# Kernel tuning notes

Hardware: AMD Instinct MI355X
Metric: run time of the kernel (lower is better)

Reference implementation:

```python
import jax, jax.numpy as jnp
import numpy as np

N_BINS = 8  # grid resolution per axis -> R = 64 regions


def setup_inputs() -> dict:
    key = jax.random.key(0)
    ks = jax.random.split(key, 11)
    N, D, A, H = 100000, 1024, 128, 256
    s = 0.02
    return {
        "x": jax.random.normal(ks[0], (N, D), dtype=jnp.float32),
        "coords": jax.random.uniform(ks[1], (N, 2), dtype=jnp.float32),
        "U_w": jax.random.normal(ks[2], (A, D), dtype=jnp.float32) * s,
        "U_b": jnp.zeros((A,), jnp.float32),
        "V_w": jax.random.normal(ks[3], (A, D), dtype=jnp.float32) * s,
        "V_b": jnp.zeros((A,), jnp.float32),
        "w_w": jax.random.normal(ks[4], (1, A), dtype=jnp.float32) * s,
        "c1_w": jax.random.normal(ks[5], (H, D), dtype=jnp.float32) * s,
        "c1_b": jnp.zeros((H,), jnp.float32),
        "c2_w": jax.random.normal(ks[6], (1, H), dtype=jnp.float32) * s,
        "c2_b": jnp.zeros((1,), jnp.float32),
    }


def reference(x, coords, U_w, U_b, V_w, V_b, w_w, c1_w, c1_b, c2_w, c2_b):
    n = N_BINS
    R = n * n
    # --- spatial binning: [N,2] coords -> [N] region ids in [0, n^2) ---
    lo = coords.min(axis=0)
    hi = coords.max(axis=0)
    span = jnp.maximum(hi - lo, 1.0)
    bins = jnp.clip(((coords - lo) / span * n).astype(jnp.int32), 0, n - 1)
    rid = bins[:, 1] * n + bins[:, 0]  # [N]
    # --- segment mean (single O(N) sweep instead of per-region loops) ---
    sums = jax.ops.segment_sum(x, rid, num_segments=R)  # [R, D]
    counts = jax.ops.segment_sum(jnp.ones((x.shape[0],), x.dtype), rid, num_segments=R)  # [R]
    r = sums / jnp.maximum(counts, 1.0)[:, None]  # [R, D], zeros for empty regions
    # --- gated attention (Ilse) over regions; empty regions masked out ---
    gate = jnp.tanh(r @ U_w.T + U_b) * jax.nn.sigmoid(r @ V_w.T + V_b)  # [R, A]
    scores = gate @ w_w.T  # [R, 1]
    scores = jnp.where(counts[:, None] > 0, scores, -jnp.inf)
    attn = jax.nn.softmax(scores, axis=0)  # [R, 1]; zero weight on empty regions
    slide = jnp.sum(attn * r, axis=0)  # [D]
    # --- classifier (dropout is identity in eval) ---
    h = jax.nn.relu(slide @ c1_w.T + c1_b)
    logit = (h @ c2_w.T + c2_b).squeeze(-1)  # scalar
    return logit, slide, attn.squeeze(-1)
```

## Files before the change

### kernel.cpp

```cpp
#include <hip/hip_runtime.h>
#include <math.h>

#define NB 8
#define NREG 64
#define DIM 1024
#define ADIM 128
#define SUBB 32

typedef float f4 __attribute__((ext_vector_type(4)));

#define SUMS_OFF  0
#define CUR_OFF   262144
#define SCORE_OFF 262400
#define PART_OFF  262656
#define SLOT_OFF  263680

__global__ __launch_bounds__(256) void k_minmax_init(const float2* __restrict__ coords,
                                                     int N,
                                                     float4* __restrict__ partial,
                                                     float* __restrict__ sums,
                                                     unsigned* __restrict__ cursor,
                                                     float* __restrict__ scores,
                                                     float* __restrict__ out,
                                                     const float* __restrict__ c2_b) {
    int b = blockIdx.x, t = threadIdx.x;
    ((float4*)sums)[b * 256 + t] = make_float4(0.f, 0.f, 0.f, 0.f);
    if (b == 0) {
        if (t < NREG) { cursor[t] = 0u; scores[t] = 0.f; }
        else if (t == 64) out[0] = c2_b[0];
    }
    float mnx = 1e30f, mny = 1e30f, mxx = -1e30f, mxy = -1e30f;
    for (int i = b * 256 + t; i < N; i += 64 * 256) {
        float2 c = coords[i];
        mnx = fminf(mnx, c.x); mny = fminf(mny, c.y);
        mxx = fmaxf(mxx, c.x); mxy = fmaxf(mxy, c.y);
    }
    for (int off = 32; off; off >>= 1) {
        mnx = fminf(mnx, __shfl_xor(mnx, off));
        mny = fminf(mny, __shfl_xor(mny, off));
        mxx = fmaxf(mxx, __shfl_xor(mxx, off));
        mxy = fmaxf(mxy, __shfl_xor(mxy, off));
    }
    __shared__ float s[4][4];
    int w = t >> 6, lane = t & 63;
    if (lane == 0) { s[w][0] = mnx; s[w][1] = mny; s[w][2] = mxx; s[w][3] = mxy; }
    __syncthreads();
    if (t == 0) {
        for (int i = 1; i < 4; ++i) {
            s[0][0] = fminf(s[0][0], s[i][0]);
            s[0][1] = fminf(s[0][1], s[i][1]);
            s[0][2] = fmaxf(s[0][2], s[i][2]);
            s[0][3] = fmaxf(s[0][3], s[i][3]);
        }
        partial[b] = make_float4(s[0][0], s[0][1], s[0][2], s[0][3]);
    }
}

__global__ __launch_bounds__(256) void k_scatter(const float2* __restrict__ coords, int N,
                                                 const float4* __restrict__ partial,
                                                 unsigned* __restrict__ cursor,
                                                 unsigned* __restrict__ slot, int cap) {
    __shared__ float prm[4];
    __shared__ unsigned lreg[NREG];
    __shared__ unsigned gbase[NREG];
    int t = threadIdx.x;
    if (t < NREG) lreg[t] = 0u;
    if (t < 64) {
        float4 p = partial[t];
        float mnx = p.x, mny = p.y, mxx = p.z, mxy = p.w;
        for (int off = 32; off; off >>= 1) {
            mnx = fminf(mnx, __shfl_xor(mnx, off));
            mny = fminf(mny, __shfl_xor(mny, off));
            mxx = fmaxf(mxx, __shfl_xor(mxx, off));
            mxy = fmaxf(mxy, __shfl_xor(mxy, off));
        }
        if (t == 0) {
            prm[0] = mnx; prm[1] = mny;
            prm[2] = fmaxf(mxx - mnx, 1.0f);
            prm[3] = fmaxf(mxy - mny, 1.0f);
        }
    }
    __syncthreads();
    int i = blockIdx.x * 256 + t;
    int r = 0; unsigned rank = 0;
    if (i < N) {
        float2 c = coords[i];
        float qx = ((c.x - prm[0]) / prm[2]) * (float)NB;
        float qy = ((c.y - prm[1]) / prm[3]) * (float)NB;
        int bx = min(max((int)qx, 0), NB - 1);
        int by = min(max((int)qy, 0), NB - 1);
        r = by * NB + bx;
        rank = atomicAdd(&lreg[r], 1u);
    }
    __syncthreads();
    if (t < NREG) gbase[t] = lreg[t] ? atomicAdd(&cursor[t], lreg[t]) : 0u;
    __syncthreads();
    if (i < N) slot[(size_t)r * cap + gbase[r] + rank] = (unsigned)i;
}

__global__ __launch_bounds__(256) void k_segsum(const f4* __restrict__ x4,
                                                const unsigned* __restrict__ slot,
                                                const unsigned* __restrict__ cursor,
                                                int cap,
                                                float* __restrict__ sums) {
    int t = threadIdx.x;
    int r = blockIdx.x & 63;
    int k = blockIdx.x >> 6;
    int cnt = (int)cursor[r];
    int chunk = ((((cnt + SUBB - 1) / SUBB) + 7) & ~7);
    int j0 = k * chunk;
    int j1 = min(cnt, j0 + chunk);
    const unsigned* sl = slot + (size_t)r * cap;

    f4 acc = (f4)(0.f);
    int j = j0;
    for (; j + 8 <= j1; j += 8) {
        uint4 ia = *(const uint4*)(sl + j);
        uint4 ib = *(const uint4*)(sl + j + 4);
        f4 v0 = x4[(size_t)ia.x * (DIM / 4) + t];
        f4 v1 = x4[(size_t)ia.y * (DIM / 4) + t];
        f4 v2 = x4[(size_t)ia.z * (DIM / 4) + t];
        f4 v3 = x4[(size_t)ia.w * (DIM / 4) + t];
        f4 v4 = x4[(size_t)ib.x * (DIM / 4) + t];
        f4 v5 = x4[(size_t)ib.y * (DIM / 4) + t];
        f4 v6 = x4[(size_t)ib.z * (DIM / 4) + t];
        f4 v7 = x4[(size_t)ib.w * (DIM / 4) + t];
        acc += v0; acc += v1; acc += v2; acc += v3;
        acc += v4; acc += v5; acc += v6; acc += v7;
    }
    for (; j < j1; ++j) {
        f4 v = x4[(size_t)sl[j] * (DIM / 4) + t];
        acc += v;
    }
    if (j1 > j0) {
        float* dst = sums + (size_t)r * DIM + 4 * t;
        unsafeAtomicAdd(dst + 0, acc.x);
        unsafeAtomicAdd(dst + 1, acc.y);
        unsafeAtomicAdd(dst + 2, acc.z);
        unsafeAtomicAdd(dst + 3, acc.w);
    }
}

__global__ __launch_bounds__(256) void k_scores(const float* __restrict__ sums,
                                                const unsigned* __restrict__ counts,
                                                const float* __restrict__ U_w,
                                                const float* __restrict__ U_b,
                                                const float* __restrict__ V_w,
                                                const float* __restrict__ V_b,
                                                const float* __restrict__ w_w,
                                                float* __restrict__ scores) {
    __shared__ float Us[4][DIM];
    __shared__ float Vs[4][DIM];
    int t = threadIdx.x, w = t >> 6, lane = t & 63;
    int q = blockIdx.x >> 1;
    int h = blockIdx.x & 1;
    int a = q * 4 + w;
    const float4* U4 = (const float4*)(U_w + (size_t)a * DIM);
    const float4* V4 = (const float4*)(V_w + (size_t)a * DIM);
    #pragma unroll
    for (int s = 0; s < 4; ++s) {
        ((float4*)Us[w])[s * 64 + lane] = U4[s * 64 + lane];
        ((float4*)Vs[w])[s * 64 + lane] = V4[s * 64 + lane];
    }
    float ub = U_b[a], vb = V_b[a], ww = w_w[a];
    int r0 = h * 32;
    for (int reg = r0; reg < r0 + 32; ++reg) {
        float inv = 1.0f / fmaxf((float)counts[reg], 1.0f);
        float du = 0.f, dv = 0.f;
        #pragma unroll
        for (int s = 0; s < 4; ++s) {
            float4 sv = ((const float4*)(sums + (size_t)reg * DIM))[s * 64 + lane];
            float4 u4 = ((const float4*)Us[w])[s * 64 + lane];
            float4 v4 = ((const float4*)Vs[w])[s * 64 + lane];
            float rx = sv.x * inv, ry = sv.y * inv, rz = sv.z * inv, rw = sv.w * inv;
            du = fmaf(u4.x, rx, fmaf(u4.y, ry, fmaf(u4.z, rz, fmaf(u4.w, rw, du))));
            dv = fmaf(v4.x, rx, fmaf(v4.y, ry, fmaf(v4.z, rz, fmaf(v4.w, rw, dv))));
        }
        for (int off = 32; off; off >>= 1) {
            du += __shfl_xor(du, off);
            dv += __shfl_xor(dv, off);
        }
        if (lane == 0) {
            float g = tanhf(du + ub) * (1.0f / (1.0f + expf(-(dv + vb))));
            unsafeAtomicAdd(&scores[reg], ww * g);
        }
    }
}

__global__ __launch_bounds__(256) void k_attn_slide(const float* __restrict__ scores,
                                                    const unsigned* __restrict__ counts,
                                                    const float* __restrict__ sums,
                                                    float* __restrict__ out) {
    __shared__ float coef[NREG];
    __shared__ float partial[4][64];
    int t = threadIdx.x;
    if (t < 64) {
        unsigned cnt = counts[t];
        float sc = (cnt > 0u) ? scores[t] : -INFINITY;
        float m = sc;
        for (int off = 32; off; off >>= 1) m = fmaxf(m, __shfl_xor(m, off));
        float e = expf(sc - m);
        float sum = e;
        for (int off = 32; off; off >>= 1) sum += __shfl_xor(sum, off);
        float a = e / sum;
        if (blockIdx.x == 0) out[1 + DIM + t] = a;
        coef[t] = a / fmaxf((float)cnt, 1.0f);
    }
    __syncthreads();
    int lane = t & 63, rg = t >> 6;
    int d = blockIdx.x * 64 + lane;
    float acc = 0.f;
    #pragma unroll
    for (int rr = 0; rr < 16; ++rr) {
        int reg = rg * 16 + rr;
        acc = fmaf(coef[reg], sums[(size_t)reg * DIM + d], acc);
    }
    partial[rg][lane] = acc;
    __syncthreads();
    if (t < 64)
        out[1 + blockIdx.x * 64 + t] =
            partial[0][t] + partial[1][t] + partial[2][t] + partial[3][t];
}

__global__ __launch_bounds__(256) void k_classifier(const float* __restrict__ c1_w,
                                                    const float* __restrict__ c1_b,
                                                    const float* __restrict__ c2_w,
                                                    const float* __restrict__ slide,
                                                    float* __restrict__ out) {
    int w = threadIdx.x >> 6, lane = threadIdx.x & 63;
    int j = blockIdx.x * 4 + w;
    const float* cw = c1_w + (size_t)j * DIM;
    float acc = 0.f;
    #pragma unroll
    for (int jj = 0; jj < 16; ++jj) {
        int d = lane + jj * 64;
        acc = fmaf(cw[d], slide[d], acc);
    }
    for (int off = 32; off; off >>= 1) acc += __shfl_xor(acc, off);
    __shared__ float sp[4];
    if (lane == 0) sp[w] = fmaxf(acc + c1_b[j], 0.f) * c2_w[j];
    __syncthreads();
    if (threadIdx.x == 0) unsafeAtomicAdd(&out[0], sp[0] + sp[1] + sp[2] + sp[3]);
}

extern "C" void kernel_launch(void* const* d_in, const int* in_sizes, int n_in,
                              void* d_out, int out_size, void* d_ws, size_t ws_size,
                              hipStream_t stream) {
    const float*  x      = (const float*)d_in[0];
    const float2* coords = (const float2*)d_in[1];
    const float*  U_w    = (const float*)d_in[2];
    const float*  U_b    = (const float*)d_in[3];
    const float*  V_w    = (const float*)d_in[4];
    const float*  V_b    = (const float*)d_in[5];
    const float*  w_w    = (const float*)d_in[6];
    const float*  c1_w   = (const float*)d_in[7];
    const float*  c1_b   = (const float*)d_in[8];
    const float*  c2_w   = (const float*)d_in[9];
    const float*  c2_b   = (const float*)d_in[10];
    int N = in_sizes[0] / DIM;

    float* out = (float*)d_out;
    char* ws = (char*)d_ws;
    float*    sums    = (float*)(ws + SUMS_OFF);
    unsigned* cursor  = (unsigned*)(ws + CUR_OFF);
    float*    scores  = (float*)(ws + SCORE_OFF);
    float4*   partial = (float4*)(ws + PART_OFF);
    unsigned* slot    = (unsigned*)(ws + SLOT_OFF);
    int cap = (N + 7) & ~7;

    hipLaunchKernelGGL(k_minmax_init, dim3(64), dim3(256), 0, stream,
                       coords, N, partial, sums, cursor, scores, out, c2_b);
    hipLaunchKernelGGL(k_scatter, dim3((N + 255) / 256), dim3(256), 0, stream,
                       coords, N, partial, cursor, slot, cap);
    hipLaunchKernelGGL(k_segsum, dim3(NREG * SUBB), dim3(256), 0, stream,
                       (const f4*)x, slot, cursor, cap, sums);
    hipLaunchKernelGGL(k_scores, dim3(64), dim3(256), 0, stream,
                       sums, cursor, U_w, U_b, V_w, V_b, w_w, scores);
    hipLaunchKernelGGL(k_attn_slide, dim3(16), dim3(256), 0, stream,
                       scores, cursor, sums, out);
    hipLaunchKernelGGL(k_classifier, dim3(NREG), dim3(256), 0, stream,
                       c1_w, c1_b, c2_w, out + 1, out);
}
```

Measured before the change: 158.6 us.

## Fuse region scatter and segment sum into per-strip shared-memory bucketing kernel

Drops the global slot index array and the separate scatter kernel. Each of 128 blocks now takes a contiguous strip of rows, bins them, counting-sorts them by region in shared memory, then streams its rows and flushes per-region partial sums to global memory with atomics. This removes one launch and the global index writes and reads, and keeps x reads local to each strip. In exchange only 128 blocks feed the bandwidth-bound sweep, and there are many more global atomic flushes, roughly one per region per strip. The shared list also caps a strip at 1024 rows.

```diff
diff --git a/kernel.cpp b/kernel.cpp
--- a/kernel.cpp
+++ b/kernel.cpp
@@ -4,29 +4,27 @@
 #define NB 8
 #define NREG 64
 #define DIM 1024
-#define ADIM 128
-#define SUBB 32
+#define STRIPS 128
 
 typedef float f4 __attribute__((ext_vector_type(4)));
 
 #define SUMS_OFF  0
-#define CUR_OFF   262144
+#define CNT_OFF   262144
 #define SCORE_OFF 262400
 #define PART_OFF  262656
-#define SLOT_OFF  263680
 
 __global__ __launch_bounds__(256) void k_minmax_init(const float2* __restrict__ coords,
                                                      int N,
                                                      float4* __restrict__ partial,
                                                      float* __restrict__ sums,
-                                                     unsigned* __restrict__ cursor,
+                                                     unsigned* __restrict__ counts,
                                                      float* __restrict__ scores,
                                                      float* __restrict__ out,
                                                      const float* __restrict__ c2_b) {
     int b = blockIdx.x, t = threadIdx.x;
     ((float4*)sums)[b * 256 + t] = make_float4(0.f, 0.f, 0.f, 0.f);
     if (b == 0) {
-        if (t < NREG) { cursor[t] = 0u; scores[t] = 0.f; }
+        if (t < NREG) { counts[t] = 0u; scores[t] = 0.f; }
         else if (t == 64) out[0] = c2_b[0];
     }
     float mnx = 1e30f, mny = 1e30f, mxx = -1e30f, mxy = -1e30f;
@@ -56,15 +54,23 @@
     }
 }
 
-__global__ __launch_bounds__(256) void k_scatter(const float2* __restrict__ coords, int N,
-                                                 const float4* __restrict__ partial,
-                                                 unsigned* __restrict__ cursor,
-                                                 unsigned* __restrict__ slot, int cap) {
+__global__ __launch_bounds__(256) void k_segsum(const f4* __restrict__ x4,
+                                                const float2* __restrict__ coords,
+                                                int N, int strip,
+                                                const float4* __restrict__ partial,
+                                                unsigned* __restrict__ counts,
+                                                float* __restrict__ sums) {
     __shared__ float prm[4];
-    __shared__ unsigned lreg[NREG];
-    __shared__ unsigned gbase[NREG];
+    __shared__ unsigned list[1024];
+    __shared__ unsigned cnt[NREG];
+    __shared__ unsigned cur[NREG];
+    __shared__ unsigned char srid[1024];
     int t = threadIdx.x;
-    if (t < NREG) lreg[t] = 0u;
+    int row0 = blockIdx.x * strip;
+    int nrows = min(N - row0, strip);
+    if (nrows <= 0) return;
+
+    if (t < NREG) cnt[t] = 0u;
     if (t < 64) {
         float4 p = partial[t];
         float mnx = p.x, mny = p.y, mxx = p.z, mxy = p.w;
@@ -81,63 +87,61 @@
         }
     }
     __syncthreads();
-    int i = blockIdx.x * 256 + t;
-    int r = 0; unsigned rank = 0;
-    if (i < N) {
-        float2 c = coords[i];
+
+    for (int p = t; p < nrows; p += 256) {
+        float2 c = coords[row0 + p];
         float qx = ((c.x - prm[0]) / prm[2]) * (float)NB;
         float qy = ((c.y - prm[1]) / prm[3]) * (float)NB;
         int bx = min(max((int)qx, 0), NB - 1);
         int by = min(max((int)qy, 0), NB - 1);
-        r = by * NB + bx;
-        rank = atomicAdd(&lreg[r], 1u);
-    }
-    __syncthreads();
-    if (t < NREG) gbase[t] = lreg[t] ? atomicAdd(&cursor[t], lreg[t]) : 0u;
-    __syncthreads();
-    if (i < N) slot[(size_t)r * cap + gbase[r] + rank] = (unsigned)i;
-}
-
-__global__ __launch_bounds__(256) void k_segsum(const f4* __restrict__ x4,
-                                                const unsigned* __restrict__ slot,
-                                                const unsigned* __restrict__ cursor,
-                                                int cap,
-                                                float* __restrict__ sums) {
-    int t = threadIdx.x;
-    int r = blockIdx.x & 63;
-    int k = blockIdx.x >> 6;
-    int cnt = (int)cursor[r];
-    int chunk = ((((cnt + SUBB - 1) / SUBB) + 7) & ~7);
-    int j0 = k * chunk;
-    int j1 = min(cnt, j0 + chunk);
-    const unsigned* sl = slot + (size_t)r * cap;
-
+        int r = by * NB + bx;
+        srid[p] = (unsigned char)r;
+        atomicAdd(&cnt[r], 1u);
+    }
+    __syncthreads();
+    if (t < NREG && cnt[t]) atomicAdd(&counts[t], cnt[t]);
+    if (t == 0) {
+        unsigned run = 0;
+        for (int i = 0; i < NREG; ++i) { cur[i] = run; run += cnt[i]; }
+    }
+    __syncthreads();
+    for (int p = t; p < nrows; p += 256) {
+        unsigned r = srid[p];
+        unsigned pos = atomicAdd(&cur[r], 1u);
+        list[pos] = (unsigned)p | (r << 16);
+    }
+    __syncthreads();
+
+    const f4* xb = x4 + (size_t)row0 * (DIM / 4) + t;
     f4 acc = (f4)(0.f);
-    int j = j0;
-    for (; j + 8 <= j1; j += 8) {
-        uint4 ia = *(const uint4*)(sl + j);
-        uint4 ib = *(const uint4*)(sl + j + 4);
-        f4 v0 = x4[(size_t)ia.x * (DIM / 4) + t];
-        f4 v1 = x4[(size_t)ia.y * (DIM / 4) + t];
-        f4 v2 = x4[(size_t)ia.z * (DIM / 4) + t];
-        f4 v3 = x4[(size_t)ia.w * (DIM / 4) + t];
-        f4 v4 = x4[(size_t)ib.x * (DIM / 4) + t];
-        f4 v5 = x4[(size_t)ib.y * (DIM / 4) + t];
-        f4 v6 = x4[(size_t)ib.z * (DIM / 4) + t];
-        f4 v7 = x4[(size_t)ib.w * (DIM / 4) + t];
-        acc += v0; acc += v1; acc += v2; acc += v3;
-        acc += v4; acc += v5; acc += v6; acc += v7;
-    }
-    for (; j < j1; ++j) {
-        f4 v = x4[(size_t)sl[j] * (DIM / 4) + t];
-        acc += v;
-    }
-    if (j1 > j0) {
-        float* dst = sums + (size_t)r * DIM + 4 * t;
-        unsafeAtomicAdd(dst + 0, acc.x);
-        unsafeAtomicAdd(dst + 1, acc.y);
-        unsafeAtomicAdd(dst + 2, acc.z);
-        unsafeAtomicAdd(dst + 3, acc.w);
+    int j = 0;
+    while (j < nrows) {
+        int take = min(8, nrows - j);
+        unsigned e[8]; f4 v[8];
+        #pragma unroll
+        for (int i = 0; i < 8; ++i) {
+            if (i < take) {
+                e[i] = list[j + i];
+                v[i] = xb[(size_t)(e[i] & 0xFFFFu) * (DIM / 4)];
+            }
+        }
+        #pragma unroll
+        for (int i = 0; i < 8; ++i) {
+            if (i < take) {
+                acc += v[i];
+                unsigned r = e[i] >> 16;
+                bool last = (j + i + 1 >= nrows) || ((list[j + i + 1] >> 16) != r);
+                if (last) {
+                    float* dst = sums + (size_t)r * DIM + 4 * t;
+                    unsafeAtomicAdd(dst + 0, acc.x);
+                    unsafeAtomicAdd(dst + 1, acc.y);
+                    unsafeAtomicAdd(dst + 2, acc.z);
+                    unsafeAtomicAdd(dst + 3, acc.w);
+                    acc = (f4)(0.f);
+                }
+            }
+        }
+        j += take;
     }
 }
 
@@ -262,22 +266,20 @@
     float* out = (float*)d_out;
     char* ws = (char*)d_ws;
     float*    sums    = (float*)(ws + SUMS_OFF);
-    unsigned* cursor  = (unsigned*)(ws + CUR_OFF);
+    unsigned* counts  = (unsigned*)(ws + CNT_OFF);
     float*    scores  = (float*)(ws + SCORE_OFF);
     float4*   partial = (float4*)(ws + PART_OFF);
-    unsigned* slot    = (unsigned*)(ws + SLOT_OFF);
-    int cap = (N + 7) & ~7;
+
+    int strip = (N + STRIPS - 1) / STRIPS;
 
     hipLaunchKernelGGL(k_minmax_init, dim3(64), dim3(256), 0, stream,
-                       coords, N, partial, sums, cursor, scores, out, c2_b);
-    hipLaunchKernelGGL(k_scatter, dim3((N + 255) / 256), dim3(256), 0, stream,
-                       coords, N, partial, cursor, slot, cap);
-    hipLaunchKernelGGL(k_segsum, dim3(NREG * SUBB), dim3(256), 0, stream,
-                       (const f4*)x, slot, cursor, cap, sums);
+                       coords, N, partial, sums, counts, scores, out, c2_b);
+    hipLaunchKernelGGL(k_segsum, dim3(STRIPS), dim3(256), 0, stream,
+                       (const f4*)x, coords, N, strip, partial, counts, sums);
     hipLaunchKernelGGL(k_scores, dim3(64), dim3(256), 0, stream,
-                       sums, cursor, U_w, U_b, V_w, V_b, w_w, scores);
+                       sums, counts, U_w, U_b, V_w, V_b, w_w, scores);
     hipLaunchKernelGGL(k_attn_slide, dim3(16), dim3(256), 0, stream,
-                       scores, cursor, sums, out);
+                       scores, counts, sums, out);
     hipLaunchKernelGGL(k_classifier, dim3(NREG), dim3(256), 0, stream,
                        c1_w, c1_b, c2_w, out + 1, out);
 }
```

Result: slower. 522.7 us (+229.7%).
